# Kernel tuning notes

Hardware: AMD Instinct MI355X
Metric: run time of the kernel (lower is better)

The kernel has to match this reference:

```python
import jax, jax.numpy as jnp
import numpy as np

B, L, E, H = 2, 2048, 2048, 16
HD = E // H  # 128
ROPE_BASE = 10000.0


def setup_inputs() -> dict:
    key = jax.random.key(0)
    k1, k2, k3 = jax.random.split(key, 3)
    x = jax.random.normal(k1, (B, L, E), dtype=jnp.float32)
    position_ids = jnp.tile(jnp.arange(L, dtype=jnp.int32)[None, :], (B, 1))
    # Linear weights stored as [in, out] so y = x @ W + b (equals torch x @ W.T + b)
    W_attn = jax.random.normal(k2, (E, 3 * E), dtype=jnp.float32) * (1.0 / np.sqrt(E))
    b_attn = jnp.zeros((3 * E,), dtype=jnp.float32)
    W_proj = jax.random.normal(k3, (E, E), dtype=jnp.float32) * (1.0 / np.sqrt(E))
    b_proj = jnp.zeros((E,), dtype=jnp.float32)
    return {"x": x, "position_ids": position_ids, "W_attn": W_attn,
            "b_attn": b_attn, "W_proj": W_proj, "b_proj": b_proj}


def _rotate_half(t):
    h = t.shape[-1] // 2
    return jnp.concatenate([-t[..., h:], t[..., :h]], axis=-1)


def _apply_rope(q, k, position_ids):
    # q,k: [B,H,L,HD]; position_ids: [B,L]
    inv_freq = 1.0 / (ROPE_BASE ** (jnp.arange(0, HD, 2, dtype=jnp.float32) / HD))
    angles = position_ids.astype(jnp.float32)[:, :, None] * inv_freq  # [B,L,HD/2]
    cos = jnp.concatenate([jnp.cos(angles)] * 2, axis=-1)[:, None]  # [B,1,L,HD]
    sin = jnp.concatenate([jnp.sin(angles)] * 2, axis=-1)[:, None]
    return q * cos + _rotate_half(q) * sin, k * cos + _rotate_half(k) * sin


def reference(x, position_ids, W_attn, b_attn, W_proj, b_proj):
    # fused QKV projection
    qkv = x @ W_attn + b_attn                       # [B,L,3E]
    q, k, v = jnp.split(qkv, 3, axis=-1)            # each [B,L,E]
    reshape = lambda t: t.reshape(B, L, H, HD).transpose(0, 2, 1, 3)  # [B,H,L,HD]
    q, k, v = reshape(q), reshape(k), reshape(v)
    q, k = _apply_rope(q, k, position_ids)
    # scaled dot-product attention (mask=None -> full attention, dropout 0)
    scores = jnp.einsum('bhqd,bhkd->bhqk', q, k) * (1.0 / np.sqrt(HD))
    probs = jax.nn.softmax(scores, axis=-1)
    y = jnp.einsum('bhqk,bhkd->bhqd', probs, v)     # [B,H,L,HD]
    y = y.transpose(0, 2, 1, 3).reshape(B, L, E)
    return y @ W_proj + b_proj
```

## Files before the change

### kernel.cpp

```cpp
#include <hip/hip_runtime.h>
#include <math.h>

#define BB 2
#define LL 2048
#define EE 2048
#define HH 16
#define HD 128
#define N3E (3*EE)

typedef __attribute__((ext_vector_type(8))) short  bf16x8;
typedef __attribute__((ext_vector_type(4))) float  f32x4;

__device__ __forceinline__ ushort f2bf(float f) {
    union { float f; unsigned u; } v; v.f = f;
    unsigned u = v.u + 0x7FFFu + ((v.u >> 16) & 1u);
    return (ushort)(u >> 16);
}
__device__ __forceinline__ float bf2f(ushort u) {
    union { unsigned u; float f; } v; v.u = ((unsigned)u) << 16;
    return v.f;
}

#define NB_CVT 4096
#define NB_T1  12288
#define NB_T2  4096

__device__ __forceinline__ void tr_block(const float* __restrict__ in,
                                         ushort* __restrict__ out,
                                         int R, int Ccol, int bx, int by,
                                         float (*tile)[33], int t) {
    int c0 = bx * 32, r0 = by * 32;
    int lr = t >> 5, lc = t & 31;
    #pragma unroll
    for (int i = 0; i < 4; ++i)
        tile[lr + i * 8][lc] = in[(size_t)(r0 + lr + i * 8) * Ccol + c0 + lc];
    __syncthreads();
    #pragma unroll
    for (int i = 0; i < 4; ++i)
        out[(size_t)(c0 + lr + i * 8) * R + r0 + lc] = f2bf(tile[lc][lr + i * 8]);
}

__global__ __launch_bounds__(256) void pre_all(const float* __restrict__ x,
                                               ushort* __restrict__ xb,
                                               const float* __restrict__ W_attn,
                                               ushort* __restrict__ Wat,
                                               const float* __restrict__ W_proj,
                                               ushort* __restrict__ Wpt) {
    __shared__ float tile[32][33];
    int bid = blockIdx.x;
    int t = threadIdx.x;
    if (bid < NB_CVT) {
        int i = (bid * 256 + t) * 8;
        float4 a = *(const float4*)(x + i);
        float4 b = *(const float4*)(x + i + 4);
        ushort4 p0 = { f2bf(a.x), f2bf(a.y), f2bf(a.z), f2bf(a.w) };
        ushort4 p1 = { f2bf(b.x), f2bf(b.y), f2bf(b.z), f2bf(b.w) };
        *(ushort4*)(xb + i)     = p0;
        *(ushort4*)(xb + i + 4) = p1;
    } else if (bid < NB_CVT + NB_T1) {
        int lb = bid - NB_CVT;
        tr_block(W_attn, Wat, EE, N3E, lb % (N3E / 32), lb / (N3E / 32), tile, t);
    } else {
        int lb = bid - NB_CVT - NB_T1;
        tr_block(W_proj, Wpt, EE, EE, lb % (EE / 32), lb / (EE / 32), tile, t);
    }
}

template<int WRITE_BF16>
__global__ __launch_bounds__(512, 2) void gemm_ktile(const ushort* __restrict__ A,
                                                     const ushort* __restrict__ Bt,
                                                     const float* __restrict__ bias,
                                                     void* __restrict__ C,
                                                     int M, int N, int K, int nbx) {
    __shared__ __align__(16) ushort Asl[4 * 8192];
    __shared__ __align__(16) ushort Bsl[4 * 4096];

    const int t    = threadIdx.x;
    const int lane = t & 63;
    const int w    = t >> 6;
    const int m    = lane & 15;
    const int quad = lane >> 4;
    const int wm   = w >> 1;
    const int wn   = w & 1;

    const int nwg = gridDim.x;
    const int cpx = nwg >> 3;
    const int swz = ((int)blockIdx.x & 7) * cpx + ((int)blockIdx.x >> 3);
    const int bx  = swz % nbx;
    const int by  = swz / nbx;
    const int m0  = by * 256, n0 = bx * 128;

    const int r16s  = (t >> 2) & 15;
    const int kels  = ((t & 3) ^ ((t & 32) ? 2 : 0)) * 8;
    const int row0s = ((t >> 6) << 4) + r16s;
    const int row1s = row0s + 128;

    const int foff = m * 32 + ((quad * 8) ^ ((m & 8) ? 16 : 0));

#define STAGE(T_) do { int _s = (T_) & 3; \
    __builtin_amdgcn_global_load_lds( \
        (const __attribute__((address_space(1))) unsigned int*)(A + (size_t)(m0 + row0s) * K + (T_) * 32 + kels), \
        (__attribute__((address_space(3))) unsigned int*)(Asl + _s * 8192 + t * 8), 16, 0, 0); \
    __builtin_amdgcn_global_load_lds( \
        (const __attribute__((address_space(1))) unsigned int*)(A + (size_t)(m0 + row1s) * K + (T_) * 32 + kels), \
        (__attribute__((address_space(3))) unsigned int*)(Asl + _s * 8192 + (512 + t) * 8), 16, 0, 0); \
    __builtin_amdgcn_global_load_lds( \
        (const __attribute__((address_space(1))) unsigned int*)(Bt + (size_t)(n0 + row0s) * K + (T_) * 32 + kels), \
        (__attribute__((address_space(3))) unsigned int*)(Bsl + _s * 4096 + t * 8), 16, 0, 0); } while (0)

    f32x4 acc[4][4];
    #pragma unroll
    for (int i = 0; i < 4; ++i)
        #pragma unroll
        for (int j = 0; j < 4; ++j) acc[i][j] = (f32x4){0.f, 0.f, 0.f, 0.f};

    const int NT = K >> 5;

    STAGE(0); STAGE(1); STAGE(2);
    asm volatile("s_waitcnt vmcnt(6)" ::: "memory");
    __builtin_amdgcn_s_barrier();

    for (int T = 0; T < NT; ++T) {
        const int slot = T & 3;
        const ushort* as = Asl + slot * 8192 + wm * 2048;
        const ushort* bs = Bsl + slot * 4096 + wn * 2048;

        bf16x8 af[4], bf[4];
        #pragma unroll
        for (int mt = 0; mt < 4; ++mt)
            af[mt] = *(const bf16x8*)(as + mt * 512 + foff);
        #pragma unroll
        for (int nt = 0; nt < 4; ++nt)
            bf[nt] = *(const bf16x8*)(bs + nt * 512 + foff);

        if (T + 3 < NT) STAGE(T + 3);

        if (T + 3 < NT)      asm volatile("s_waitcnt vmcnt(6)" ::: "memory");
        else if (T + 2 < NT) asm volatile("s_waitcnt vmcnt(3)" ::: "memory");
        else                 asm volatile("s_waitcnt vmcnt(0)" ::: "memory");
        __builtin_amdgcn_s_barrier();
        asm volatile("s_waitcnt lgkmcnt(0)" ::: "memory");
        __builtin_amdgcn_s_setprio(1);
        #pragma unroll
        for (int mt = 0; mt < 4; ++mt)
            #pragma unroll
            for (int nt = 0; nt < 4; ++nt)
                acc[mt][nt] = __builtin_amdgcn_mfma_f32_16x16x32_bf16(af[mt], bf[nt], acc[mt][nt], 0, 0, 0);
        __builtin_amdgcn_s_setprio(0);
        __builtin_amdgcn_s_barrier();
    }
#undef STAGE

    float bcol[4];
    #pragma unroll
    for (int nt = 0; nt < 4; ++nt) bcol[nt] = bias[n0 + wn * 64 + nt * 16 + m];
    #pragma unroll
    for (int mt = 0; mt < 4; ++mt) {
        #pragma unroll
        for (int nt = 0; nt < 4; ++nt) {
            #pragma unroll
            for (int r = 0; r < 4; ++r) {
                int row = m0 + wm * 64 + mt * 16 + quad * 4 + r;
                int col = n0 + wn * 64 + nt * 16 + m;
                float v = acc[mt][nt][r] + bcol[nt];
                if (WRITE_BF16) ((ushort*)C)[(size_t)row * N + col] = f2bf(v);
                else            ((float*)C)[(size_t)row * N + col] = v;
            }
        }
    }
}

__global__ __launch_bounds__(256) void prep_qkv(const ushort* __restrict__ qkvb,
                                                const int* __restrict__ pos_ids,
                                                ushort* __restrict__ Qt,
                                                ushort* __restrict__ Kt,
                                                ushort* __restrict__ Vtt) {
    __shared__ ushort vlds[64 * 136];
    int bid = blockIdx.x;
    int t   = threadIdx.x;

    if (bid < 4096) {
        const float scale = 0.08838834764831845f;
        const float nl2b = -0.20762050593046014f;
        int idx = bid * 256 + t;
        int p    = idx & 15;
        int r    = (idx >> 4) & 63;
        int tile = (idx >> 10) & 31;
        int h    = (idx >> 15) & 15;
        int b    = idx >> 19;
        int c    = p ^ (r & 15);
        int l    = tile * 64 + r;
        int half = c >> 3, cl = c & 7;
        const ushort* row = qkvb + (size_t)(b * LL + l) * N3E;
        float pos = (float)pos_ids[b * LL + l];

        bf16x8 qa = *(const bf16x8*)(row + h * HD + c * 8);
        bf16x8 qb = *(const bf16x8*)(row + h * HD + (c ^ 8) * 8);
        bf16x8 ka = *(const bf16x8*)(row + EE + h * HD + c * 8);
        bf16x8 kb = *(const bf16x8*)(row + EE + h * HD + (c ^ 8) * 8);
        bf16x8 qo, ko;
        #pragma unroll
        for (int i = 0; i < 8; ++i) {
            int j = cl * 8 + i;
            float ang = pos * exp2f((float)j * nl2b);
            float s, cs;
            sincosf(ang, &s, &cs);
            float sgn = half ? s : -s;
            float q1 = bf2f((ushort)qa[i]), q2 = bf2f((ushort)qb[i]);
            float k1 = bf2f((ushort)ka[i]), k2 = bf2f((ushort)kb[i]);
            qo[i] = (short)f2bf((q1 * cs + q2 * sgn) * scale);
            ko[i] = (short)f2bf(k1 * cs + k2 * sgn);
        }
        size_t obase = ((size_t)(b * 16 + h) * 32 + tile) * 8192 + r * 128 + p * 8;
        *(bf16x8*)(Qt + obase) = qo;
        *(bf16x8*)(Kt + obase) = ko;
    } else {
        int vb   = bid - 4096;
        int tile = vb & 31;
        int bh   = vb >> 5;
        int b    = bh >> 4, h = bh & 15;

        #pragma unroll
        for (int it = 0; it < 4; ++it) {
            int c4 = t + it * 256;
            int kk = c4 >> 4, dc = c4 & 15;
            bf16x8 v = *(const bf16x8*)(qkvb + (size_t)(b * LL + tile * 64 + kk) * N3E
                                        + 2 * EE + h * HD + dc * 8);
            int colp = (dc * 8) ^ ((kk >> 3) << 4);
            *(bf16x8*)(vlds + kk * 136 + colp) = v;
        }
        __syncthreads();
        #pragma unroll
        for (int it = 0; it < 4; ++it) {
            int oc = t + it * 256;
            int p = oc & 7, r = oc >> 3;
            int c = p ^ (r & 7);
            bf16x8 o;
            #pragma unroll
            for (int i = 0; i < 8; ++i) {
                int kk = c * 8 + i;
                o[i] = (short)vlds[kk * 136 + (r ^ ((kk >> 3) << 4))];
            }
            *(bf16x8*)(Vtt + ((size_t)bh * 32 + tile) * 8192 + r * 64 + p * 8) = o;
        }
    }
}

#define PSTR 68

__global__ __launch_bounds__(256, 2) void flash2(const ushort* __restrict__ Qt,
                                                 const ushort* __restrict__ Kt,
                                                 const ushort* __restrict__ Vtt,
                                                 ushort* __restrict__ y) {
    __shared__ __align__(16) ushort Ps[4 * 32 * PSTR];

    const int t    = threadIdx.x;
    const int w    = t >> 6;
    const int lane = t & 63;
    const int m    = lane & 15;
    const int quad = lane >> 4;
    const int qblk = blockIdx.x;
    const int bh   = blockIdx.y;
    const int b    = bh >> 4, h = bh & 15;

    const ushort* Qhead = Qt  + (size_t)bh * 32 * 8192;
    const ushort* Khead = Kt  + (size_t)bh * 32 * 8192;
    const ushort* Vhead = Vtt + (size_t)bh * 32 * 8192;

    bf16x8 qf[2][4];
    #pragma unroll
    for (int mt = 0; mt < 2; ++mt) {
        int rloc = w * 32 + mt * 16 + m;
        const ushort* qtile = Qhead + (size_t)(qblk * 2 + (rloc >> 6)) * 8192
                              + (rloc & 63) * 128;
        #pragma unroll
        for (int ks = 0; ks < 4; ++ks)
            qf[mt][ks] = *(const bf16x8*)(qtile + ((ks * 4 + quad) ^ m) * 8);
    }

    f32x4 oacc[2][8];
    #pragma unroll
    for (int mt = 0; mt < 2; ++mt)
        #pragma unroll
        for (int dt = 0; dt < 8; ++dt) oacc[mt][dt] = (f32x4){0.f, 0.f, 0.f, 0.f};
    float m_i[8], l_pl[8];
    #pragma unroll
    for (int s = 0; s < 8; ++s) { m_i[s] = -INFINITY; l_pl[s] = 0.f; }

    for (int kt = 0; kt < 32; ++kt) {
        const ushort* ktile = Khead + (size_t)kt * 8192;
        const ushort* vtile = Vhead + (size_t)kt * 8192;

        f32x4 sacc[2][4];
        #pragma unroll
        for (int mt = 0; mt < 2; ++mt)
            #pragma unroll
            for (int nt = 0; nt < 4; ++nt) sacc[mt][nt] = (f32x4){0.f, 0.f, 0.f, 0.f};
        #pragma unroll
        for (int ks = 0; ks < 4; ++ks) {
            #pragma unroll
            for (int nt = 0; nt < 4; ++nt) {
                bf16x8 kf = *(const bf16x8*)(ktile + (nt * 16 + m) * 128
                                             + (((ks * 4 + quad) ^ m)) * 8);
                sacc[0][nt] = __builtin_amdgcn_mfma_f32_16x16x32_bf16(qf[0][ks], kf, sacc[0][nt], 0, 0, 0);
                sacc[1][nt] = __builtin_amdgcn_mfma_f32_16x16x32_bf16(qf[1][ks], kf, sacc[1][nt], 0, 0, 0);
            }
        }

        float alpha_s[2][4];
        #pragma unroll
        for (int mt = 0; mt < 2; ++mt) {
            #pragma unroll
            for (int r = 0; r < 4; ++r) {
                int slot = mt * 4 + r;
                float mx = fmaxf(fmaxf(sacc[mt][0][r], sacc[mt][1][r]),
                                 fmaxf(sacc[mt][2][r], sacc[mt][3][r]));
                #pragma unroll
                for (int off = 1; off < 16; off <<= 1) mx = fmaxf(mx, __shfl_xor(mx, off, 64));
                float mnew = fmaxf(m_i[slot], mx);
                float al = __expf(m_i[slot] - mnew);
                m_i[slot] = mnew;
                float rs = 0.f;
                #pragma unroll
                for (int nt = 0; nt < 4; ++nt) {
                    float pv = __expf(sacc[mt][nt][r] - mnew);
                    sacc[mt][nt][r] = pv;
                    rs += pv;
                }
                l_pl[slot] = l_pl[slot] * al + rs;
                alpha_s[mt][r] = al;
            }
        }
        #pragma unroll
        for (int mt = 0; mt < 2; ++mt)
            #pragma unroll
            for (int dt = 0; dt < 8; ++dt)
                #pragma unroll
                for (int r = 0; r < 4; ++r) oacc[mt][dt][r] *= alpha_s[mt][r];

        #pragma unroll
        for (int mt = 0; mt < 2; ++mt)
            #pragma unroll
            for (int nt = 0; nt < 4; ++nt)
                #pragma unroll
                for (int r = 0; r < 4; ++r)
                    Ps[w * 32 * PSTR + (mt * 16 + quad * 4 + r) * PSTR + nt * 16 + m]
                        = f2bf(sacc[mt][nt][r]);

        #pragma unroll
        for (int ks2 = 0; ks2 < 2; ++ks2) {
            bf16x8 pf0 = *(const bf16x8*)&Ps[w * 32 * PSTR + (0 * 16 + m) * PSTR + ks2 * 32 + quad * 8];
            bf16x8 pf1 = *(const bf16x8*)&Ps[w * 32 * PSTR + (1 * 16 + m) * PSTR + ks2 * 32 + quad * 8];
            #pragma unroll
            for (int dt = 0; dt < 8; ++dt) {
                bf16x8 vf = *(const bf16x8*)(vtile + (dt * 16 + m) * 64
                                             + (((ks2 * 4 + quad) ^ (m & 7))) * 8);
                oacc[0][dt] = __builtin_amdgcn_mfma_f32_16x16x32_bf16(pf0, vf, oacc[0][dt], 0, 0, 0);
                oacc[1][dt] = __builtin_amdgcn_mfma_f32_16x16x32_bf16(pf1, vf, oacc[1][dt], 0, 0, 0);
            }
        }
    }

    #pragma unroll
    for (int s = 0; s < 8; ++s) {
        #pragma unroll
        for (int off = 1; off < 16; off <<= 1) l_pl[s] += __shfl_xor(l_pl[s], off, 64);
        l_pl[s] = 1.0f / l_pl[s];
    }
    #pragma unroll
    for (int mt = 0; mt < 2; ++mt) {
        #pragma unroll
        for (int dt = 0; dt < 8; ++dt) {
            #pragma unroll
            for (int r = 0; r < 4; ++r) {
                int row = qblk * 128 + w * 32 + mt * 16 + quad * 4 + r;
                y[(size_t)(b * LL + row) * EE + h * HD + dt * 16 + m]
                    = f2bf(oacc[mt][dt][r] * l_pl[mt * 4 + r]);
            }
        }
    }
}

extern "C" void kernel_launch(void* const* d_in, const int* in_sizes, int n_in,
                              void* d_out, int out_size, void* d_ws, size_t ws_size,
                              hipStream_t stream) {
    const float* x      = (const float*)d_in[0];
    const int*   pos    = (const int*)d_in[1];
    const float* W_attn = (const float*)d_in[2];
    const float* b_attn = (const float*)d_in[3];
    const float* W_proj = (const float*)d_in[4];
    const float* b_proj = (const float*)d_in[5];
    float* out = (float*)d_out;

    const int M = BB * LL;
    ushort* xb   = (ushort*)d_ws;
    ushort* Wat  = xb   + (size_t)M * EE;
    ushort* Wpt  = Wat  + (size_t)N3E * EE;
    ushort* qkvb = Wpt  + (size_t)EE * EE;
    ushort* Kt   = qkvb + (size_t)M * N3E;
    ushort* Vtt  = Kt   + (size_t)M * EE;
    ushort* Qt   = xb;
    ushort* yb   = Wat;

    pre_all<<<dim3(NB_CVT + NB_T1 + NB_T2), dim3(256), 0, stream>>>(
        x, xb, W_attn, Wat, W_proj, Wpt);

    gemm_ktile<1><<<dim3((M / 256) * (N3E / 128)), dim3(512), 0, stream>>>(
        xb, Wat, b_attn, qkvb, M, N3E, EE, N3E / 128);

    prep_qkv<<<dim3(4096 + 1024), dim3(256), 0, stream>>>(qkvb, pos, Qt, Kt, Vtt);

    flash2<<<dim3(LL / 128, BB * HH), dim3(256), 0, stream>>>(Qt, Kt, Vtt, yb);

    gemm_ktile<0><<<dim3((M / 256) * (EE / 128)), dim3(512), 0, stream>>>(
        yb, Wpt, b_proj, out, M, EE, EE, EE / 128);
}
```

Before: 453.9 us.

## Pre-pack Q/K/V tiles in MFMA fragment order for contiguous per-lane loads

```diff
diff --git a/kernel.cpp b/kernel.cpp
--- a/kernel.cpp
+++ b/kernel.cpp
@@ -182,13 +182,16 @@
     if (bid < 4096) {
         const float scale = 0.08838834764831845f;
         const float nl2b = -0.20762050593046014f;
-        int idx = bid * 256 + t;
-        int p    = idx & 15;
-        int r    = (idx >> 4) & 63;
+        int idx  = bid * 256 + t;
+        int m    = idx & 15;
+        int quad = (idx >> 4) & 3;
+        int ks   = (idx >> 6) & 3;
+        int nt   = (idx >> 8) & 3;
         int tile = (idx >> 10) & 31;
         int h    = (idx >> 15) & 15;
         int b    = idx >> 19;
-        int c    = p ^ (r & 15);
+        int c    = ks * 4 + quad;
+        int r    = nt * 16 + m;
         int l    = tile * 64 + r;
         int half = c >> 3, cl = c & 7;
         const ushort* row = qkvb + (size_t)(b * LL + l) * N3E;
@@ -211,7 +214,8 @@
             qo[i] = (short)f2bf((q1 * cs + q2 * sgn) * scale);
             ko[i] = (short)f2bf(k1 * cs + k2 * sgn);
         }
-        size_t obase = ((size_t)(b * 16 + h) * 32 + tile) * 8192 + r * 128 + p * 8;
+        size_t obase = ((size_t)(b * 16 + h) * 32 + tile) * 8192
+                       + (nt * 4 + ks) * 512 + (quad * 16 + m) * 8;
         *(bf16x8*)(Qt + obase) = qo;
         *(bf16x8*)(Kt + obase) = ko;
     } else {
@@ -230,18 +234,22 @@
             *(bf16x8*)(vlds + kk * 136 + colp) = v;
         }
         __syncthreads();
+        size_t tbase = ((size_t)bh * 32 + tile) * 8192;
         #pragma unroll
         for (int it = 0; it < 4; ++it) {
-            int oc = t + it * 256;
-            int p = oc & 7, r = oc >> 3;
-            int c = p ^ (r & 7);
+            int oc   = t + it * 256;
+            int m    = oc & 15;
+            int quad = (oc >> 4) & 3;
+            int ks2  = (oc >> 6) & 1;
+            int dt   = (oc >> 7) & 7;
+            int d    = dt * 16 + m;
+            int kkb  = (ks2 * 4 + quad) * 8;
+            int msk  = (ks2 * 4 + quad) << 4;
             bf16x8 o;
             #pragma unroll
-            for (int i = 0; i < 8; ++i) {
-                int kk = c * 8 + i;
-                o[i] = (short)vlds[kk * 136 + (r ^ ((kk >> 3) << 4))];
-            }
-            *(bf16x8*)(Vtt + ((size_t)bh * 32 + tile) * 8192 + r * 64 + p * 8) = o;
+            for (int i = 0; i < 8; ++i)
+                o[i] = (short)vlds[(kkb + i) * 136 + (d ^ msk)];
+            *(bf16x8*)(Vtt + tbase + (dt * 2 + ks2) * 512 + (quad * 16 + m) * 8) = o;
         }
     }
 }
@@ -268,14 +276,15 @@
     const ushort* Vhead = Vtt + (size_t)bh * 32 * 8192;
 
     bf16x8 qf[2][4];
-    #pragma unroll
-    for (int mt = 0; mt < 2; ++mt) {
-        int rloc = w * 32 + mt * 16 + m;
-        const ushort* qtile = Qhead + (size_t)(qblk * 2 + (rloc >> 6)) * 8192
-                              + (rloc & 63) * 128;
-        #pragma unroll
-        for (int ks = 0; ks < 4; ++ks)
-            qf[mt][ks] = *(const bf16x8*)(qtile + ((ks * 4 + quad) ^ m) * 8);
+    {
+        const ushort* qtile = Qhead + (size_t)(qblk * 2 + (w >> 1)) * 8192;
+        #pragma unroll
+        for (int mt = 0; mt < 2; ++mt) {
+            int ntq = (w & 1) * 2 + mt;
+            #pragma unroll
+            for (int ks = 0; ks < 4; ++ks)
+                qf[mt][ks] = *(const bf16x8*)(qtile + (ntq * 4 + ks) * 512 + lane * 8);
+        }
     }
 
     f32x4 oacc[2][8];
@@ -300,8 +309,7 @@
         for (int ks = 0; ks < 4; ++ks) {
             #pragma unroll
             for (int nt = 0; nt < 4; ++nt) {
-                bf16x8 kf = *(const bf16x8*)(ktile + (nt * 16 + m) * 128
-                                             + (((ks * 4 + quad) ^ m)) * 8);
+                bf16x8 kf = *(const bf16x8*)(ktile + (nt * 4 + ks) * 512 + lane * 8);
                 sacc[0][nt] = __builtin_amdgcn_mfma_f32_16x16x32_bf16(qf[0][ks], kf, sacc[0][nt], 0, 0, 0);
                 sacc[1][nt] = __builtin_amdgcn_mfma_f32_16x16x32_bf16(qf[1][ks], kf, sacc[1][nt], 0, 0, 0);
             }
@@ -353,8 +361,7 @@
             bf16x8 pf1 = *(const bf16x8*)&Ps[w * 32 * PSTR + (1 * 16 + m) * PSTR + ks2 * 32 + quad * 8];
             #pragma unroll
             for (int dt = 0; dt < 8; ++dt) {
-                bf16x8 vf = *(const bf16x8*)(vtile + (dt * 16 + m) * 64
-                                             + (((ks2 * 4 + quad) ^ (m & 7))) * 8);
+                bf16x8 vf = *(const bf16x8*)(vtile + (dt * 2 + ks2) * 512 + lane * 8);
                 oacc[0][dt] = __builtin_amdgcn_mfma_f32_16x16x32_bf16(pf0, vf, oacc[0][dt], 0, 0, 0);
                 oacc[1][dt] = __builtin_amdgcn_mfma_f32_16x16x32_bf16(pf1, vf, oacc[1][dt], 0, 0, 0);
             }
```

Result: slower. 468.3 us (+3.2%).
